# Kernel tuning notes

Hardware: AMD Instinct MI355X
Metric: run time of the kernel (lower is better)

## Reference

```python
import jax, jax.numpy as jnp
import numpy as np

H, KV, D, HID, FF = 32, 8, 128, 4096, 14336
EPS = 1e-5
ROPE_THETA = 1e9


def setup_inputs() -> dict:
    key = jax.random.key(0)
    ks = jax.random.split(key, 10)
    B, S = 1, 2048
    s = 0.02
    return {
        "hidden_states": jax.random.normal(ks[0], (B, S, HID), dtype=jnp.float32),
        "wq": jax.random.normal(ks[1], (HID, H * D), dtype=jnp.float32) * s,
        "wk": jax.random.normal(ks[2], (HID, KV * D), dtype=jnp.float32) * s,
        "wv": jax.random.normal(ks[3], (HID, KV * D), dtype=jnp.float32) * s,
        "wo": jax.random.normal(ks[4], (H * D, HID), dtype=jnp.float32) * s,
        "w_gate": jax.random.normal(ks[5], (HID, FF), dtype=jnp.float32) * s,
        "w_up": jax.random.normal(ks[6], (HID, FF), dtype=jnp.float32) * s,
        "w_down": jax.random.normal(ks[7], (FF, HID), dtype=jnp.float32) * s,
        "ln1_w": jnp.ones((HID,), dtype=jnp.float32),
        "ln2_w": jnp.ones((HID,), dtype=jnp.float32),
        "position_ids": jnp.arange(B * S, dtype=jnp.int32).reshape(B, S),
    }


def _rmsnorm(x, w):
    var = jnp.mean(jnp.square(x), axis=-1, keepdims=True)
    return x * jax.lax.rsqrt(var + EPS) * w


def _rope_cos_sin(position_ids):
    inv_freq = 1.0 / (ROPE_THETA ** (jnp.arange(0, D, 2, dtype=jnp.float32) / D))  # [D/2]
    ang = position_ids.astype(jnp.float32)[..., None] * inv_freq  # [B,S,D/2]
    ang = jnp.concatenate([ang, ang], axis=-1)  # [B,S,D]
    return jnp.cos(ang), jnp.sin(ang)


def _rotate_half(x):
    x1, x2 = x[..., : D // 2], x[..., D // 2:]
    return jnp.concatenate([-x2, x1], axis=-1)


def _apply_rope(x, cos, sin):
    # x: [B,S,h,D]; cos/sin: [B,S,D]
    c, s = cos[:, :, None, :], sin[:, :, None, :]
    return x * c + _rotate_half(x) * s


def reference(hidden_states, wq, wk, wv, wo, w_gate, w_up, w_down, ln1_w, ln2_w, position_ids):
    B, S, _ = hidden_states.shape
    G = H // KV  # query groups per kv head

    # --- attention block ---
    residual = hidden_states
    x = _rmsnorm(hidden_states, ln1_w)
    q = (x @ wq).reshape(B, S, H, D)
    k = (x @ wk).reshape(B, S, KV, D)
    v = (x @ wv).reshape(B, S, KV, D)

    cos, sin = _rope_cos_sin(position_ids)
    q = _apply_rope(q, cos, sin)
    k = _apply_rope(k, cos, sin)

    # GQA: group query heads over kv heads, [B,S,KV,G,D]
    qg = q.reshape(B, S, KV, G, D)
    scores = jnp.einsum("bqhgd,bkhd->bhgqk", qg, k) / jnp.sqrt(jnp.float32(D))
    causal = position_ids[:, :, None] >= position_ids[:, None, :]  # [B,S,S]
    scores = jnp.where(causal[:, None, None, :, :], scores, jnp.float32(-1e9))
    probs = jax.nn.softmax(scores, axis=-1)
    attn = jnp.einsum("bhgqk,bkhd->bqhgd", probs, v).reshape(B, S, H * D)
    hidden_states = residual + attn @ wo

    # --- MLP block (SwiGLU) ---
    residual = hidden_states
    x = _rmsnorm(hidden_states, ln2_w)
    mlp = (jax.nn.silu(x @ w_gate) * (x @ w_up)) @ w_down
    return residual + mlp
```

## Files before the change

kernel.cpp:

```cpp
#include <hip/hip_runtime.h>

typedef short bf16x8 __attribute__((ext_vector_type(8)));
typedef float f32x4 __attribute__((ext_vector_type(4)));

#define DEV __device__ __forceinline__

constexpr int SEQ = 2048;
constexpr int HID = 4096;
constexpr int NH  = 32;
constexpr int NKV = 8;
constexpr int DH  = 128;
constexpr int FF  = 14336;
constexpr int QKVN = NH * DH + 2 * NKV * DH;

DEV unsigned short f2bf(float f) {
  union { float f; unsigned u; } x; x.f = f;
  unsigned r = x.u + 0x7fffu + ((x.u >> 16) & 1u);
  return (unsigned short)(r >> 16);
}
DEV float bf2f(unsigned short u) {
  union { unsigned u; float f; } x; x.u = ((unsigned)u) << 16; return x.f;
}
DEV void gload16(const void* g, void* l) {
  __builtin_amdgcn_global_load_lds(
      (const __attribute__((address_space(1))) unsigned*)g,
      (__attribute__((address_space(3))) unsigned*)l, 16, 0, 0);
}

DEV void wtrans_tail(char* smbase, int tid, int tile0, int stride,
                     const float* __restrict__ TW,
                     unsigned short* __restrict__ TWT, int TK, int TN) {
  const int team = tid >> 8, lt = tid & 255;
  unsigned short(*tt)[72] = (unsigned short(*)[72])(smbase + team * 9216);
  const int tilesK = TK >> 6;
  const int tot = tilesK * (TN >> 6);
  const int tk = lt >> 4;
  const int tn4 = (lt & 15) * 4;
  for (int tile = tile0 * 2 + team; tile < tot; tile += stride * 2) {
    const int k0 = (tile % tilesK) << 6;
    const int n0t = (tile / tilesK) << 6;
#pragma unroll
    for (int p = 0; p < 4; ++p) {
      int k = tk + p * 16;
      float4 v = *(const float4*)(TW + (size_t)(k0 + k) * TN + n0t + tn4);
      tt[tn4 + 0][k] = f2bf(v.x);
      tt[tn4 + 1][k] = f2bf(v.y);
      tt[tn4 + 2][k] = f2bf(v.z);
      tt[tn4 + 3][k] = f2bf(v.w);
    }
    __syncthreads();
#pragma unroll
    for (int p = 0; p < 4; ++p) {
      int n = tk + p * 16;
      ushort4 o = *(const ushort4*)&tt[n][tn4];
      *(ushort4*)(TWT + (size_t)(n0t + n) * TK + k0 + tn4) = o;
    }
    __syncthreads();
  }
}

__global__ __launch_bounds__(256) void rmsnorm_kernel(
    const float* __restrict__ x, const float* __restrict__ w,
    unsigned short* __restrict__ out) {
  const int row = blockIdx.x;
  const int tid = threadIdx.x;
  const float* xr = x + (size_t)row * HID;
  float4 v[4];
  float ss = 0.f;
#pragma unroll
  for (int i = 0; i < 4; ++i) {
    v[i] = *(const float4*)(xr + i * 1024 + tid * 4);
    ss += v[i].x * v[i].x + v[i].y * v[i].y + v[i].z * v[i].z + v[i].w * v[i].w;
  }
#pragma unroll
  for (int m = 1; m < 64; m <<= 1) ss += __shfl_xor(ss, m);
  __shared__ float red[4];
  if ((tid & 63) == 0) red[tid >> 6] = ss;
  __syncthreads();
  float tot = red[0] + red[1] + red[2] + red[3];
  float rms = rsqrtf(tot / (float)HID + 1e-5f);
  unsigned short* orow = out + (size_t)row * HID;
#pragma unroll
  for (int i = 0; i < 4; ++i) {
    int base = i * 1024 + tid * 4;
    ushort4 o;
    o.x = f2bf(v[i].x * rms * w[base + 0]);
    o.y = f2bf(v[i].y * rms * w[base + 1]);
    o.z = f2bf(v[i].z * rms * w[base + 2]);
    o.w = f2bf(v[i].w * rms * w[base + 3]);
    *(ushort4*)(orow + base) = o;
  }
}

__global__ __launch_bounds__(256) void wtrans_kernel(
    const float* __restrict__ W, unsigned short* __restrict__ WT, int K,
    int N) {
  __shared__ unsigned short t[64][72];
  const int k0 = blockIdx.x * 64, n0 = blockIdx.y * 64;
  const int tid = threadIdx.x;
  const int tk = tid >> 4;
  const int tn4 = (tid & 15) * 4;
#pragma unroll
  for (int p = 0; p < 4; ++p) {
    int k = tk + p * 16;
    float4 v = *(const float4*)(W + (size_t)(k0 + k) * N + n0 + tn4);
    t[tn4 + 0][k] = f2bf(v.x);
    t[tn4 + 1][k] = f2bf(v.y);
    t[tn4 + 2][k] = f2bf(v.z);
    t[tn4 + 3][k] = f2bf(v.w);
  }
  __syncthreads();
#pragma unroll
  for (int p = 0; p < 4; ++p) {
    int n = tk + p * 16;
    ushort4 o = *(const ushort4*)&t[n][tn4];
    *(ushort4*)(WT + (size_t)(n0 + n) * K + k0 + tn4) = o;
  }
}

__global__ __launch_bounds__(256) void rope_kernel(unsigned short* __restrict__ x,
                                                   int nheads, int ld) {
  const int gid = blockIdx.x * 256 + threadIdx.x;
  const int i = gid & 63;
  const int t = gid >> 6;
  const int s = t / nheads;
  const int hh = t - s * nheads;
  float ang = (float)s * exp2f((float)i * (-29.897352853986263f / 64.f));
  float sn, cs;
  sincosf(ang, &sn, &cs);
  size_t base = (size_t)s * ld + hh * DH + i;
  float x1 = bf2f(x[base]);
  float x2 = bf2f(x[base + 64]);
  x[base]      = f2bf(x1 * cs - x2 * sn);
  x[base + 64] = f2bf(x2 * cs + x1 * sn);
}

__global__ __launch_bounds__(256) void combine_kernel(
    const float* __restrict__ p0, const float* __restrict__ p1,
    const float* __restrict__ res, float* __restrict__ out) {
  const size_t i = ((size_t)blockIdx.x * 256 + threadIdx.x) * 4;
  float4 a = *(const float4*)(p0 + i);
  float4 b = *(const float4*)(p1 + i);
  float4 c = *(const float4*)(res + i);
  float4 o;
  o.x = a.x + b.x + c.x;
  o.y = a.y + b.y + c.y;
  o.z = a.z + b.z + c.z;
  o.w = a.w + b.w + c.w;
  *(float4*)(out + i) = o;
}

__global__ __launch_bounds__(256) void combine_rms_kernel(
    const float* __restrict__ p0, const float* __restrict__ p1,
    const float* __restrict__ res, const float* __restrict__ w,
    float* __restrict__ h2, unsigned short* __restrict__ xn2) {
  const int row = blockIdx.x;
  const int tid = threadIdx.x;
  const size_t base = (size_t)row * HID;
  float4 h[4];
  float ss = 0.f;
#pragma unroll
  for (int i = 0; i < 4; ++i) {
    size_t idx = base + i * 1024 + tid * 4;
    float4 a = *(const float4*)(p0 + idx);
    float4 b = *(const float4*)(p1 + idx);
    float4 c = *(const float4*)(res + idx);
    h[i].x = a.x + b.x + c.x;
    h[i].y = a.y + b.y + c.y;
    h[i].z = a.z + b.z + c.z;
    h[i].w = a.w + b.w + c.w;
    *(float4*)(h2 + idx) = h[i];
    ss += h[i].x * h[i].x + h[i].y * h[i].y + h[i].z * h[i].z + h[i].w * h[i].w;
  }
#pragma unroll
  for (int m = 1; m < 64; m <<= 1) ss += __shfl_xor(ss, m);
  __shared__ float red[4];
  if ((tid & 63) == 0) red[tid >> 6] = ss;
  __syncthreads();
  float tot = red[0] + red[1] + red[2] + red[3];
  float rms = rsqrtf(tot / (float)HID + 1e-5f);
#pragma unroll
  for (int i = 0; i < 4; ++i) {
    int off = i * 1024 + tid * 4;
    ushort4 o;
    o.x = f2bf(h[i].x * rms * w[off + 0]);
    o.y = f2bf(h[i].y * rms * w[off + 1]);
    o.z = f2bf(h[i].z * rms * w[off + 2]);
    o.w = f2bf(h[i].w * rms * w[off + 3]);
    *(ushort4*)(xn2 + base + off) = o;
  }
}

template <int EPI>
__global__ __launch_bounds__(512, 2) void gemm8p_kernel(
    const unsigned short* __restrict__ A, const unsigned short* __restrict__ BT,
    void* __restrict__ Cv0, void* __restrict__ Cv1, int gridM, int N, int Kld,
    int nsplit, const float* __restrict__ TW, unsigned short* __restrict__ TWT,
    int TK, int TN, int n_t) {
  constexpr int MF = 4;
  constexpr int ABYTES = 256 * 128;
  constexpr int BUFBYTES = ABYTES + 32768;
  __shared__ __align__(128) char sm[2 * BUFBYTES];

  const int tid = threadIdx.x;
  const int nwg = gridDim.x - n_t;

  if ((int)blockIdx.x >= nwg) {
    wtrans_tail(sm, tid, (int)blockIdx.x - nwg, n_t, TW, TWT, TK, TN);
    return;
  }

  const int lane = tid & 63;
  const int wv   = tid >> 6;
  const int b = blockIdx.x;
  const int logical = (b & 7) * (nwg >> 3) + (b >> 3);
  const int ntiles = nwg / nsplit;
  const int s = logical / ntiles;
  const int r = logical - s * ntiles;
  const int m0 = (r % gridM) * 256;
  const int n0 = (r / gridM) * 256;
  const int Klen = Kld / nsplit;
  const int koff = s * Klen;
  const int wm = (wv >> 2) * 128;
  const int wn = (wv & 3) * 64;
  const int nt = Klen >> 6;

  const int srow = tid >> 3;
  const int scolb = (tid & 7) * 16;
  const int sldsbase = wv * 1024;

  auto stage = [&](int h, int t) {
    const int buf = t & 1;
    const int kt = koff + t * 64;
    char* ldsOp;
    const unsigned short* g;
    int grow0, rowBase;
    if (h < 2) {
      ldsOp = sm + buf * BUFBYTES + ABYTES; g = BT; grow0 = n0; rowBase = h * 128;
    } else {
      ldsOp = sm + buf * BUFBYTES;          g = A;  grow0 = m0; rowBase = (h - 2) * 128;
    }
#pragma unroll
    for (int rr = 0; rr < 2; ++rr) {
      int row = rowBase + rr * 64 + srow;
      const char* gp = (const char*)g + ((size_t)(grow0 + row) * Kld + kt) * 2 +
                       (scolb ^ ((row & 7) << 4));
      gload16(gp, ldsOp + rowBase * 128 + rr * 8192 + sldsbase);
    }
  };

  const int kb0 = (lane >> 4) * 16;
  const int lrow = lane & 15;
  auto ldA = [&](const char* sA, int mh, int mf, int ks) {
    int row = wm + mh * 64 + mf * 16 + lrow;
    return *(const bf16x8*)(sA + ((row * 128 + kb0 + ks * 64) ^ ((row & 7) << 4)));
  };
  auto ldB = [&](const char* sB, int j, int ks) {
    int col = wn + j * 16 + lrow;
    return *(const bf16x8*)(sB + ((col * 128 + kb0 + ks * 64) ^ ((col & 7) << 4)));
  };

  f32x4 acc[2 * MF][4] = {};

  stage(2, 0); stage(3, 0); stage(0, 0); stage(1, 0);
  if (nt > 1) {
    stage(0, 1); stage(1, 1);
    asm volatile("s_waitcnt vmcnt(4)" ::: "memory");
  } else {
    asm volatile("s_waitcnt vmcnt(0)" ::: "memory");
  }
  __builtin_amdgcn_s_barrier();

  for (int t = 0; t < nt; ++t) {
    const char* sA = sm + (t & 1) * BUFBYTES;
    const char* sB = sA + ABYTES;
    bf16x8 a[MF], bb[4][2];

#pragma unroll
    for (int j = 0; j < 4; ++j) bb[j][0] = ldB(sB, j, 0);
#pragma unroll
    for (int mf = 0; mf < MF; ++mf) a[mf] = ldA(sA, 0, mf, 0);
    if (t + 1 < nt) stage(2, t + 1);
    __builtin_amdgcn_sched_barrier(0);
    __builtin_amdgcn_s_barrier();
    __builtin_amdgcn_s_setprio(1);
#pragma unroll
    for (int mf = 0; mf < MF; ++mf)
#pragma unroll
      for (int j = 0; j < 4; ++j)
        acc[mf][j] = __builtin_amdgcn_mfma_f32_16x16x32_bf16(
            a[mf], bb[j][0], acc[mf][j], 0, 0, 0);
    __builtin_amdgcn_s_setprio(0);
    __builtin_amdgcn_sched_barrier(0);
    __builtin_amdgcn_s_barrier();

#pragma unroll
    for (int j = 0; j < 4; ++j) bb[j][1] = ldB(sB, j, 1);
#pragma unroll
    for (int mf = 0; mf < MF; ++mf) a[mf] = ldA(sA, 0, mf, 1);
    if (t + 1 < nt) stage(3, t + 1);
    __builtin_amdgcn_sched_barrier(0);
    __builtin_amdgcn_s_barrier();
    __builtin_amdgcn_s_setprio(1);
#pragma unroll
    for (int mf = 0; mf < MF; ++mf)
#pragma unroll
      for (int j = 0; j < 4; ++j)
        acc[mf][j] = __builtin_amdgcn_mfma_f32_16x16x32_bf16(
            a[mf], bb[j][1], acc[mf][j], 0, 0, 0);
    __builtin_amdgcn_s_setprio(0);
    __builtin_amdgcn_sched_barrier(0);
    __builtin_amdgcn_s_barrier();

#pragma unroll
    for (int mf = 0; mf < MF; ++mf) a[mf] = ldA(sA, 1, mf, 0);
    if (t + 2 < nt) stage(0, t + 2);
    __builtin_amdgcn_sched_barrier(0);
    __builtin_amdgcn_s_barrier();
    __builtin_amdgcn_s_setprio(1);
#pragma unroll
    for (int mf = 0; mf < MF; ++mf)
#pragma unroll
      for (int j = 0; j < 4; ++j)
        acc[MF + mf][j] = __builtin_amdgcn_mfma_f32_16x16x32_bf16(
            a[mf], bb[j][0], acc[MF + mf][j], 0, 0, 0);
    __builtin_amdgcn_s_setprio(0);
    __builtin_amdgcn_sched_barrier(0);
    __builtin_amdgcn_s_barrier();

#pragma unroll
    for (int mf = 0; mf < MF; ++mf) a[mf] = ldA(sA, 1, mf, 1);
    if (t + 2 < nt) {
      stage(1, t + 2);
      asm volatile("s_waitcnt vmcnt(4)" ::: "memory");
    } else {
      asm volatile("s_waitcnt vmcnt(0)" ::: "memory");
    }
    __builtin_amdgcn_sched_barrier(0);
    __builtin_amdgcn_s_barrier();
    __builtin_amdgcn_s_setprio(1);
#pragma unroll
    for (int mf = 0; mf < MF; ++mf)
#pragma unroll
      for (int j = 0; j < 4; ++j)
        acc[MF + mf][j] = __builtin_amdgcn_mfma_f32_16x16x32_bf16(
            a[mf], bb[j][1], acc[MF + mf][j], 0, 0, 0);
    __builtin_amdgcn_s_setprio(0);
    __builtin_amdgcn_sched_barrier(0);
    __builtin_amdgcn_s_barrier();
  }

  const int rb = (lane >> 4) * 4;
  float* P = (float*)(s ? Cv1 : Cv0);
#pragma unroll
  for (int i = 0; i < 2 * MF; ++i) {
    const int mh = i / MF, mf = i % MF;
#pragma unroll
    for (int j = 0; j < 4; ++j) {
#pragma unroll
      for (int rr = 0; rr < 4; ++rr) {
        size_t row = (size_t)(m0 + wm + mh * 64 + mf * 16 + rb + rr);
        size_t col = (size_t)(n0 + wn + j * 16 + lrow);
        float vv = acc[i][j][rr];
        if (EPI == 0) {
          ((unsigned short*)Cv0)[row * N + col] = f2bf(vv);
        } else if (EPI == 2) {
          P[row * N + col] = vv;
        } else {
          float g = bf2f(((const unsigned short*)Cv1)[row * N + col]);
          float sl = g / (1.f + __expf(-g));
          ((unsigned short*)Cv0)[row * N + col] = f2bf(sl * vv);
        }
      }
    }
  }
}

__global__ __launch_bounds__(512, 1) void attn_kernel(
    const unsigned short* __restrict__ QKV, unsigned short* __restrict__ Ob,
    const float* __restrict__ TW, unsigned short* __restrict__ TWT, int TK,
    int TN, int n_t) {
  __shared__ __align__(128) char sm[131072];
  const int tid  = threadIdx.x;
  const int nattn = gridDim.x - n_t;
  if ((int)blockIdx.x >= nattn) {
    wtrans_tail(sm, tid, (int)blockIdx.x - nattn, n_t, TW, TWT, TK, TN);
    return;
  }
  char* sQ  = sm;
  char* sKb = sm + 32768;
  char* sVb = sm + 81920;
  char* sP  = sm + 114688;
  const int lane = tid & 63;
  const int wv   = tid >> 6;
  const int logical = blockIdx.x;
  const int xr = 15 - (logical >> 5);
  const int h = logical & 31;
  const int qb0 = xr * 128;
  const int hkv = h >> 2;
  const int rbase = (lane >> 4) * 4;
  const int cbase = lane & 15;
  const unsigned short* Qp = QKV + h * DH;
  const unsigned short* Kp = QKV + NH * DH + hkv * DH;
  const unsigned short* Vp = QKV + NH * DH + NKV * DH + hkv * DH;

#pragma unroll
  for (int i = 0; i < 4; ++i) {
    int offs = i * 8192 + tid * 16;
    int row = offs >> 8, col = offs & 255;
    const char* gp = (const char*)Qp + ((size_t)(qb0 + row) * QKVN) * 2 +
                     (col ^ ((row & 15) << 4));
    gload16(gp, sQ + i * 8192 + wv * 1024);
  }

  auto stageK = [&](int t) {
    char* dst = sKb + (t % 3) * 16384;
    const int kt0 = t * 64;
#pragma unroll
    for (int i = 0; i < 2; ++i) {
      int offs = i * 8192 + tid * 16;
      int row = offs >> 8, col = offs & 255;
      const char* gp = (const char*)Kp + ((size_t)(kt0 + row) * QKVN) * 2 +
                       (col ^ ((row & 15) << 4));
      gload16(gp, dst + i * 8192 + wv * 1024);
    }
  };

  const int d4  = (tid & 31) * 4;
  const int kv4 = (tid >> 5) * 4;
  const int rot = (tid >> 1) & 3;
  auto loadV = [&](int t, ushort4* vr) {
    const unsigned short* g0 = Vp + (size_t)(t * 64 + kv4) * QKVN + d4;
#pragma unroll
    for (int k = 0; k < 4; ++k) vr[k] = *(const ushort4*)(g0 + (size_t)k * QKVN);
  };
  auto writeV = [&](int t, const ushort4* vr) {
    char* dst = sVb + (t & 1) * 16384;
    const unsigned short* a0 = (const unsigned short*)&vr[0];
    const unsigned short* a1 = (const unsigned short*)&vr[1];
    const unsigned short* a2 = (const unsigned short*)&vr[2];
    const unsigned short* a3 = (const unsigned short*)&vr[3];
#pragma unroll
    for (int j = 0; j < 4; ++j) {
      int jj = (j + rot) & 3;
      int dd = d4 + jj;
      uint2 pk;
      pk.x = (unsigned)a0[jj] | ((unsigned)a1[jj] << 16);
      pk.y = (unsigned)a2[jj] | ((unsigned)a3[jj] << 16);
      *(uint2*)(dst + ((dd * 128 + kv4 * 2) ^ ((dd & 7) << 4))) = pk;
    }
  };

  const int ntiles = 2 * (xr + 1);
  ushort4 vr[4];
  stageK(0);
  loadV(0, vr);
  asm volatile("s_waitcnt vmcnt(0)" ::: "memory");
  writeV(0, vr);
  if (ntiles > 1) stageK(1);
  __syncthreads();

  const int qrow = wv * 16 + (lane & 15);
  bf16x8 aq[4];
#pragma unroll
  for (int kk = 0; kk < 4; ++kk) {
    int kb = (lane >> 4) * 16 + kk * 64;
    aq[kk] = *(const bf16x8*)(sQ + ((qrow * 256 + kb) ^ ((qrow & 15) << 4)));
  }

  f32x4 oacc[8] = {};
  float m_r[4] = {-1e30f, -1e30f, -1e30f, -1e30f};
  float l_r[4] = {0.f, 0.f, 0.f, 0.f};

  for (int t = 0; t < ntiles; ++t) {
    const int kt0 = t * 64;
    const char* cK = sKb + (t % 3) * 16384;
    const char* cV = sVb + (t & 1) * 16384;
    if (t + 1 < ntiles) loadV(t + 1, vr);
    if (t + 2 < ntiles) stageK(t + 2);

    f32x4 sacc[4] = {};
#pragma unroll
    for (int kk = 0; kk < 4; ++kk) {
      int kb = (lane >> 4) * 16 + kk * 64;
#pragma unroll
      for (int ni = 0; ni < 4; ++ni) {
        int krow = ni * 16 + (lane & 15);
        bf16x8 bk =
            *(const bf16x8*)(cK + ((krow * 256 + kb) ^ ((krow & 15) << 4)));
        sacc[ni] = __builtin_amdgcn_mfma_f32_16x16x32_bf16(aq[kk], bk,
                                                           sacc[ni], 0, 0, 0);
      }
    }

    const float scale = 0.08838834764831845f;
    float sfv[4];
    bool anyresc = false;
#pragma unroll
    for (int r = 0; r < 4; ++r) {
      int qg = qb0 + wv * 16 + rbase + r;
      float mx = -1e30f;
#pragma unroll
      for (int ni = 0; ni < 4; ++ni) {
        int cg = kt0 + ni * 16 + cbase;
        float sv = sacc[ni][r] * scale;
        sv = (cg <= qg) ? sv : -1e30f;
        sacc[ni][r] = sv;
        mx = fmaxf(mx, sv);
      }
      mx = fmaxf(mx, __shfl_xor(mx, 1));
      mx = fmaxf(mx, __shfl_xor(mx, 2));
      mx = fmaxf(mx, __shfl_xor(mx, 4));
      mx = fmaxf(mx, __shfl_xor(mx, 8));
      bool grew = mx > m_r[r] + 5.0f;
      float mnew = grew ? mx : m_r[r];
      float sf = grew ? __expf(m_r[r] - mnew) : 1.0f;
      sfv[r] = sf;
      anyresc |= grew;
      m_r[r] = mnew;
      float rsum = 0.f;
#pragma unroll
      for (int ni = 0; ni < 4; ++ni) {
        float pv = __expf(sacc[ni][r] - mnew);
        sacc[ni][r] = pv;
        rsum += pv;
      }
      rsum += __shfl_xor(rsum, 1);
      rsum += __shfl_xor(rsum, 2);
      rsum += __shfl_xor(rsum, 4);
      rsum += __shfl_xor(rsum, 8);
      l_r[r] = l_r[r] * sf + rsum;
    }
    if (__any(anyresc)) {
#pragma unroll
      for (int nt2 = 0; nt2 < 8; ++nt2)
#pragma unroll
        for (int r = 0; r < 4; ++r) oacc[nt2][r] *= sfv[r];
    }

    char* pw = sP + wv * 2048;
#pragma unroll
    for (int ni = 0; ni < 4; ++ni)
#pragma unroll
      for (int r = 0; r < 4; ++r) {
        int row = rbase + r;
        int cb2 = (ni * 16 + cbase) * 2;
        *(unsigned short*)(pw + ((row * 128 + cb2) ^ ((row & 7) << 4))) =
            f2bf(sacc[ni][r]);
      }
    asm volatile("s_waitcnt lgkmcnt(0)" ::: "memory");

#pragma unroll
    for (int kk = 0; kk < 2; ++kk) {
      int kb = (lane >> 4) * 16 + kk * 64;
      int prow = lane & 15;
      bf16x8 ap =
          *(const bf16x8*)(pw + ((prow * 128 + kb) ^ ((prow & 7) << 4)));
#pragma unroll
      for (int nt2 = 0; nt2 < 8; ++nt2) {
        int vrow = nt2 * 16 + (lane & 15);
        bf16x8 bv =
            *(const bf16x8*)(cV + ((vrow * 128 + kb) ^ ((vrow & 7) << 4)));
        oacc[nt2] =
            __builtin_amdgcn_mfma_f32_16x16x32_bf16(ap, bv, oacc[nt2], 0, 0, 0);
      }
    }

    if (t + 1 < ntiles) {
      if (t + 2 < ntiles)
        asm volatile("s_waitcnt vmcnt(2)" ::: "memory");
      else
        asm volatile("s_waitcnt vmcnt(0)" ::: "memory");
      writeV(t + 1, vr);
    }
    __syncthreads();
  }

#pragma unroll
  for (int nt2 = 0; nt2 < 8; ++nt2)
#pragma unroll
    for (int r = 0; r < 4; ++r) {
      size_t row = (size_t)(qb0 + wv * 16 + rbase + r);
      int col = nt2 * 16 + cbase;
      Ob[row * (NH * DH) + h * DH + col] = f2bf(oacc[nt2][r] / l_r[r]);
    }
}

extern "C" void kernel_launch(void* const* d_in, const int* in_sizes, int n_in,
                              void* d_out, int out_size, void* d_ws,
                              size_t ws_size, hipStream_t stream) {
  const float* hs  = (const float*)d_in[0];
  const float* wq  = (const float*)d_in[1];
  const float* wk  = (const float*)d_in[2];
  const float* wvp = (const float*)d_in[3];
  const float* wo  = (const float*)d_in[4];
  const float* wg  = (const float*)d_in[5];
  const float* wu  = (const float*)d_in[6];
  const float* wd  = (const float*)d_in[7];
  const float* ln1 = (const float*)d_in[8];
  const float* ln2 = (const float*)d_in[9];

  char* p = (char*)d_ws;
  size_t need = 0;
  auto alloc = [&](size_t bytes) {
    char* r = p + need;
    need += (bytes + 255) & ~(size_t)255;
    return r;
  };
  unsigned short* T1   = (unsigned short*)alloc((size_t)FF * HID * 2);
  unsigned short* xn   = (unsigned short*)alloc((size_t)SEQ * HID * 2);
  unsigned short* qkv  = (unsigned short*)alloc((size_t)SEQ * QKVN * 2);
  unsigned short* ab   = (unsigned short*)alloc((size_t)SEQ * NH * DH * 2);
  float*          h2   = (float*)alloc((size_t)SEQ * HID * 4);
  unsigned short* xn2  = (unsigned short*)alloc((size_t)SEQ * HID * 2);
  unsigned short* gbuf = (unsigned short*)alloc((size_t)SEQ * FF * 2);
  unsigned short* ubuf = (unsigned short*)alloc((size_t)SEQ * FF * 2);
  size_t need_base = need;
  unsigned short* T2   = (unsigned short*)alloc((size_t)FF * HID * 2);
  const bool fat = (ws_size >= need);
  if (ws_size < need_base) return;

  float* pO0 = (float*)gbuf;
  float* pO1 = (float*)xn;
  float* pD0 = fat ? (float*)T2 : (float*)ubuf;
  float* pD1 = fat ? (float*)(T2 + (size_t)SEQ * HID * 2) : (float*)xn;
  (void)ubuf;

  rmsnorm_kernel<<<SEQ, 256, 0, stream>>>(hs, ln1, xn);
  wtrans_kernel<<<dim3(HID / 64, HID / 64), 256, 0, stream>>>(wq, T1, HID, HID);
  wtrans_kernel<<<dim3(HID / 64, (NKV * DH) / 64), 256, 0, stream>>>(
      wk, T1 + (size_t)(NH * DH) * HID, HID, NKV * DH);
  wtrans_kernel<<<dim3(HID / 64, (NKV * DH) / 64), 256, 0, stream>>>(
      wvp, T1 + (size_t)(NH * DH + NKV * DH) * HID, HID, NKV * DH);
  if (fat) {
    gemm8p_kernel<0><<<192 + 64, 512, 0, stream>>>(
        xn, T1, qkv, nullptr, SEQ / 256, QKVN, HID, 1, wo, T2, HID, HID, 64);
  } else {
    gemm8p_kernel<0><<<192, 512, 0, stream>>>(
        xn, T1, qkv, nullptr, SEQ / 256, QKVN, HID, 1, nullptr, nullptr, 64, 64, 0);
  }
  rope_kernel<<<(SEQ * (NH + NKV) * 64) / 256, 256, 0, stream>>>(qkv, NH + NKV,
                                                                 QKVN);
  if (fat) {
    attn_kernel<<<512 + 512, 512, 0, stream>>>(qkv, ab, wg, T1, HID, FF, 512);
  } else {
    attn_kernel<<<512, 512, 0, stream>>>(qkv, ab, nullptr, nullptr, 64, 64, 0);
  }
  unsigned short* Wo = fat ? T2 : T1;
  if (!fat)
    wtrans_kernel<<<dim3(HID / 64, HID / 64), 256, 0, stream>>>(wo, T1, HID, HID);
  gemm8p_kernel<2><<<256, 512, 0, stream>>>(
      ab, Wo, pO0, pO1, SEQ / 256, HID, HID, 2, nullptr, nullptr, 64, 64, 0);
  combine_rms_kernel<<<SEQ, 256, 0, stream>>>(pO0, pO1, hs, ln2, h2, xn2);
  if (fat) {
    gemm8p_kernel<0><<<448 + 64, 512, 0, stream>>>(
        xn2, T1, gbuf, nullptr, SEQ / 256, FF, HID, 1, wu, T2, HID, FF, 64);
  } else {
    wtrans_kernel<<<dim3(HID / 64, FF / 64), 256, 0, stream>>>(wg, T1, HID, FF);
    gemm8p_kernel<0><<<448, 512, 0, stream>>>(
        xn2, T1, gbuf, nullptr, SEQ / 256, FF, HID, 1, nullptr, nullptr, 64, 64, 0);
  }
  if (fat) {
    gemm8p_kernel<3><<<448 + 64, 512, 0, stream>>>(
        xn2, T2, gbuf, gbuf, SEQ / 256, FF, HID, 1, wd, T1, FF, HID, 64);
  } else {
    wtrans_kernel<<<dim3(HID / 64, FF / 64), 256, 0, stream>>>(wu, T1, HID, FF);
    gemm8p_kernel<3><<<448, 512, 0, stream>>>(
        xn2, T1, gbuf, gbuf, SEQ / 256, FF, HID, 1, nullptr, nullptr, 64, 64, 0);
  }
  if (!fat)
    wtrans_kernel<<<dim3(FF / 64, HID / 64), 256, 0, stream>>>(wd, T1, FF, HID);
  gemm8p_kernel<2><<<256, 512, 0, stream>>>(
      gbuf, T1, pD0, pD1, SEQ / 256, HID, FF, 2, nullptr, nullptr, 64, 64, 0);
  combine_kernel<<<(SEQ * HID) / 1024, 256, 0, stream>>>(pD0, pD1, h2,
                                                         (float*)d_out);
}
```

Baseline: 1.357 ms.

## Overlap gate and up weight transposes with attention, transpose down weights separately

The attention launch's extra blocks now transpose both the gate and the up weights, split in half between the two, instead of only the gate weights. The wo transpose is redirected into the gbuf buffer during the QKV GEMM, and the partial-output buffer moves to ubuf. The gate and up GEMMs no longer carry piggybacked transpose blocks. The down-weight transpose becomes a standalone kernel after the gate GEMM. The aim is to fill idle CUs during the causal, load-imbalanced attention with more transpose work, at the cost of exposing the down-weight transpose as its own launch.

After: 1.317 ms. 2.9% less time.

```diff
diff --git a/kernel.cpp b/kernel.cpp
--- a/kernel.cpp
+++ b/kernel.cpp
@@ -378,13 +378,19 @@
 
 __global__ __launch_bounds__(512, 1) void attn_kernel(
     const unsigned short* __restrict__ QKV, unsigned short* __restrict__ Ob,
-    const float* __restrict__ TW, unsigned short* __restrict__ TWT, int TK,
-    int TN, int n_t) {
+    const float* __restrict__ TW1, unsigned short* __restrict__ TWT1,
+    const float* __restrict__ TW2, unsigned short* __restrict__ TWT2,
+    int n_t) {
   __shared__ __align__(128) char sm[131072];
   const int tid  = threadIdx.x;
   const int nattn = gridDim.x - n_t;
   if ((int)blockIdx.x >= nattn) {
-    wtrans_tail(sm, tid, (int)blockIdx.x - nattn, n_t, TW, TWT, TK, TN);
+    const int ti = (int)blockIdx.x - nattn;
+    const int half = n_t >> 1;
+    if (ti < half)
+      wtrans_tail(sm, tid, ti, half, TW1, TWT1, HID, FF);
+    else
+      wtrans_tail(sm, tid, ti - half, half, TW2, TWT2, HID, FF);
     return;
   }
   char* sQ  = sm;
@@ -620,11 +626,10 @@
   const bool fat = (ws_size >= need);
   if (ws_size < need_base) return;
 
-  float* pO0 = (float*)gbuf;
+  float* pO0 = (float*)ubuf;
   float* pO1 = (float*)xn;
   float* pD0 = fat ? (float*)T2 : (float*)ubuf;
   float* pD1 = fat ? (float*)(T2 + (size_t)SEQ * HID * 2) : (float*)xn;
-  (void)ubuf;
 
   rmsnorm_kernel<<<SEQ, 256, 0, stream>>>(hs, ln1, xn);
   wtrans_kernel<<<dim3(HID / 64, HID / 64), 256, 0, stream>>>(wq, T1, HID, HID);
@@ -634,7 +639,8 @@
       wvp, T1 + (size_t)(NH * DH + NKV * DH) * HID, HID, NKV * DH);
   if (fat) {
     gemm8p_kernel<0><<<192 + 64, 512, 0, stream>>>(
-        xn, T1, qkv, nullptr, SEQ / 256, QKVN, HID, 1, wo, T2, HID, HID, 64);
+        xn, T1, qkv, nullptr, SEQ / 256, QKVN, HID, 1, wo, (unsigned short*)gbuf,
+        HID, HID, 64);
   } else {
     gemm8p_kernel<0><<<192, 512, 0, stream>>>(
         xn, T1, qkv, nullptr, SEQ / 256, QKVN, HID, 1, nullptr, nullptr, 64, 64, 0);
@@ -642,34 +648,31 @@
   rope_kernel<<<(SEQ * (NH + NKV) * 64) / 256, 256, 0, stream>>>(qkv, NH + NKV,
                                                                  QKVN);
   if (fat) {
-    attn_kernel<<<512 + 512, 512, 0, stream>>>(qkv, ab, wg, T1, HID, FF, 512);
+    attn_kernel<<<512 + 1024, 512, 0, stream>>>(qkv, ab, wg, T1, wu, T2, 1024);
   } else {
-    attn_kernel<<<512, 512, 0, stream>>>(qkv, ab, nullptr, nullptr, 64, 64, 0);
-  }
-  unsigned short* Wo = fat ? T2 : T1;
+    attn_kernel<<<512, 512, 0, stream>>>(qkv, ab, nullptr, nullptr, nullptr,
+                                         nullptr, 0);
+  }
+  unsigned short* Wo = fat ? (unsigned short*)gbuf : T1;
   if (!fat)
     wtrans_kernel<<<dim3(HID / 64, HID / 64), 256, 0, stream>>>(wo, T1, HID, HID);
   gemm8p_kernel<2><<<256, 512, 0, stream>>>(
       ab, Wo, pO0, pO1, SEQ / 256, HID, HID, 2, nullptr, nullptr, 64, 64, 0);
   combine_rms_kernel<<<SEQ, 256, 0, stream>>>(pO0, pO1, hs, ln2, h2, xn2);
+  if (!fat)
+    wtrans_kernel<<<dim3(HID / 64, FF / 64), 256, 0, stream>>>(wg, T1, HID, FF);
+  gemm8p_kernel<0><<<448, 512, 0, stream>>>(
+      xn2, T1, gbuf, nullptr, SEQ / 256, FF, HID, 1, nullptr, nullptr, 64, 64, 0);
+  wtrans_kernel<<<dim3(FF / 64, HID / 64), 256, 0, stream>>>(wd, T1, FF, HID);
   if (fat) {
-    gemm8p_kernel<0><<<448 + 64, 512, 0, stream>>>(
-        xn2, T1, gbuf, nullptr, SEQ / 256, FF, HID, 1, wu, T2, HID, FF, 64);
-  } else {
-    wtrans_kernel<<<dim3(HID / 64, FF / 64), 256, 0, stream>>>(wg, T1, HID, FF);
-    gemm8p_kernel<0><<<448, 512, 0, stream>>>(
-        xn2, T1, gbuf, nullptr, SEQ / 256, FF, HID, 1, nullptr, nullptr, 64, 64, 0);
-  }
-  if (fat) {
-    gemm8p_kernel<3><<<448 + 64, 512, 0, stream>>>(
-        xn2, T2, gbuf, gbuf, SEQ / 256, FF, HID, 1, wd, T1, FF, HID, 64);
+    gemm8p_kernel<3><<<448, 512, 0, stream>>>(
+        xn2, T2, gbuf, gbuf, SEQ / 256, FF, HID, 1, nullptr, nullptr, 64, 64, 0);
   } else {
     wtrans_kernel<<<dim3(HID / 64, FF / 64), 256, 0, stream>>>(wu, T1, HID, FF);
     gemm8p_kernel<3><<<448, 512, 0, stream>>>(
         xn2, T1, gbuf, gbuf, SEQ / 256, FF, HID, 1, nullptr, nullptr, 64, 64, 0);
-  }
-  if (!fat)
     wtrans_kernel<<<dim3(FF / 64, HID / 64), 256, 0, stream>>>(wd, T1, FF, HID);
+  }
   gemm8p_kernel<2><<<256, 512, 0, stream>>>(
       gbuf, T1, pD0, pD1, SEQ / 256, HID, FF, 2, nullptr, nullptr, 64, 64, 0);
   combine_kernel<<<(SEQ * HID) / 1024, 256, 0, stream>>>(pD0, pD1, h2,
```
